# Kernel tuning notes

Hardware: AMD Instinct MI355X
Metric: run time of the kernel (lower is better)

The kernel has to match this reference:

```python
import jax, jax.numpy as jnp
import numpy as np

N, E, B = 100000, 3200000, 1024
D_LM, K, H, C, L = 1024, 128, 256, 40, 2
T = 0.1
LN_EPS = 1e-5


def _layernorm(x, g, b):
    m = x.mean(-1, keepdims=True)
    v = ((x - m) ** 2).mean(-1, keepdims=True)
    return (x - m) * jax.lax.rsqrt(v + LN_EPS) * g + b


def _gcn_conv(x, W, b, src, dst, norm, self_w):
    h = x @ W
    agg = jax.ops.segment_sum(h[src] * norm[:, None], dst, num_segments=N)
    return agg + h * self_w[:, None] + b


def setup_inputs() -> dict:
    key = jax.random.key(0)
    ks = jax.random.split(key, 20)
    s = 0.02
    rn = lambda k, shp: jax.random.normal(k, shp, jnp.float32) * s
    return {
        "hidden_embeds": jax.random.normal(ks[0], (L, N, D_LM), jnp.float32),
        "proj_W1": rn(ks[1], (L, D_LM, K)),
        "proj_b1": jnp.zeros((L, K), jnp.float32),
        "ln_g": jnp.ones((L, K), jnp.float32),
        "ln_b": jnp.zeros((L, K), jnp.float32),
        "proj_W2": rn(ks[2], (L, K, K)),
        "proj_b2": jnp.zeros((L, K), jnp.float32),
        "alphas": jnp.zeros((L,), jnp.float32),
        "gcn_W1": rn(ks[3], (L, K, H)),
        "gcn_b1": jnp.zeros((L, H), jnp.float32),
        "gcn_W2": rn(ks[4], (L, H, K)),
        "gcn_b2": jnp.zeros((L, K), jnp.float32),
        "clf_W": rn(ks[5], (2 * K, C)),
        "clf_b": jnp.zeros((C,), jnp.float32),
        "edge_index": jax.random.randint(ks[6], (2, E), 0, N, jnp.int64 if jax.config.jax_enable_x64 else jnp.int32),
        "mapping": jax.random.randint(ks[7], (B,), 0, N, jnp.int64 if jax.config.jax_enable_x64 else jnp.int32),
    }


def reference(hidden_embeds, proj_W1, proj_b1, ln_g, ln_b, proj_W2, proj_b2,
              alphas, gcn_W1, gcn_b1, gcn_W2, gcn_b2, clf_W, clf_b,
              edge_index, mapping):
    src, dst = edge_index[0], edge_index[1]
    ones = jnp.ones((E,), jnp.float32)
    # GCN normalization (self loops included): deg over dst + 1
    deg = jax.ops.segment_sum(ones, dst, num_segments=N) + 1.0
    dis = jax.lax.rsqrt(deg)
    norm = dis[src] * dis[dst]          # per-edge D^-1/2 A D^-1/2
    self_w = 1.0 / deg                  # self-loop weight dis[i]*dis[i]

    last = None
    for i in range(L):
        # projector: Linear -> LayerNorm -> ReLU -> Linear
        h = hidden_embeds[i] @ proj_W1[i] + proj_b1[i]
        h = jax.nn.relu(_layernorm(h, ln_g[i], ln_b[i]))
        h = h @ proj_W2[i] + proj_b2[i]
        if i > 0:
            a = jax.nn.sigmoid(alphas[i] / T)
            h = h * a + last * (1.0 - a)
        # 2-layer GCN encoder (dropout=0)
        z = jax.nn.relu(_gcn_conv(h, gcn_W1[i], gcn_b1[i], src, dst, norm, self_w))
        last = _gcn_conv(z, gcn_W2[i], gcn_b2[i], src, dst, norm, self_w)

    # custom_global_mean_pool: mean over {node} U {out-neighbors} U {in-neighbors}
    sum_n = (jax.ops.segment_sum(last[dst], src, num_segments=N)
             + jax.ops.segment_sum(last[src], dst, num_segments=N))
    cnt = (jax.ops.segment_sum(ones, src, num_segments=N)
           + jax.ops.segment_sum(ones, dst, num_segments=N))
    pooled = (last[mapping] + sum_n[mapping]) / (1.0 + cnt[mapping])[:, None]

    out = jnp.concatenate([last[mapping], pooled], axis=1)  # [B, 2K]
    return out @ clf_W + clf_b
```

## Files before the change

kernel.cpp:

```cpp
#include <hip/hip_runtime.h>
#include <hip/hip_bf16.h>
#include <math.h>

using short8 = __attribute__((ext_vector_type(8))) short;
using f32x4  = __attribute__((ext_vector_type(4))) float;

#define PSTRIDE 2048

__device__ __forceinline__ short f2bf(float f) {
    __hip_bfloat16 h = __float2bfloat16(f);
    return *reinterpret_cast<short*>(&h);
}


__global__ void map_scatter_k(const int* __restrict__ mapping, int* __restrict__ map_idx, int B)
{
    int b = blockIdx.x * blockDim.x + threadIdx.x;
    if (b < B) map_idx[mapping[b]] = b;
}

__launch_bounds__(1024)
__global__ void bin_count_k(const int* __restrict__ dst, int E, int* __restrict__ bin_cnt)
{
    __shared__ int h[4096];
    for (int i = threadIdx.x; i < 4096; i += 1024) h[i] = 0;
    __syncthreads();
    int base = blockIdx.x * 32768;
#pragma unroll
    for (int i = 0; i < 32; ++i) {
        int e = base + i * 1024 + threadIdx.x;
        if (e < E) atomicAdd(&h[dst[e] >> 5], 1);
    }
    __syncthreads();
    for (int i = threadIdx.x; i < 4096; i += 1024) {
        int c = h[i];
        if (c) atomicAdd(&bin_cnt[i], c);
    }
}

__launch_bounds__(1024)
__global__ void scan_bins_k(const int* __restrict__ cnt, int* __restrict__ off,
                            int* __restrict__ cur)
{
    __shared__ int wsum[16];
    int tid = threadIdx.x, lane = tid & 63, wid = tid >> 6;
    int4 v = ((const int4*)cnt)[tid];
    int s0 = v.x, s1 = s0 + v.y, s2 = s1 + v.z, s3 = s2 + v.w;
    int q = s3;
#pragma unroll
    for (int o = 1; o < 64; o <<= 1) { int t = __shfl_up(q, o); if (lane >= o) q += t; }
    if (lane == 63) wsum[wid] = q;
    __syncthreads();
    if (wid == 0) {
        int w = (lane < 16) ? wsum[lane] : 0;
#pragma unroll
        for (int o = 1; o < 16; o <<= 1) { int t = __shfl_up(w, o); if (lane >= o) w += t; }
        if (lane < 16) wsum[lane] = w;
    }
    __syncthreads();
    int base = (wid ? wsum[wid - 1] : 0) + q - s3;
    int4 o4; o4.x = base; o4.y = base + s0; o4.z = base + s1; o4.w = base + s2;
    ((int4*)off)[tid] = o4;
    ((int4*)cur)[tid] = o4;
    if (tid == 1023) off[4096] = base + s3;
}

__launch_bounds__(256)
__global__ void bin_scatter_k(const int* __restrict__ ei, int E,
                              const int* __restrict__ map_idx,
                              int* __restrict__ bin_cur, unsigned* __restrict__ pairs,
                              int* __restrict__ pcnt, int* __restrict__ pnb)
{
    int e = blockIdx.x * blockDim.x + threadIdx.x;
    if (e >= E) return;
    int s = ei[e];
    int d = ei[E + e];
    int p = atomicAdd(&bin_cur[d >> 5], 1);
    pairs[p] = (unsigned)s | ((unsigned)(d & 31) << 27);
    int ms = map_idx[s];
    if (ms >= 0) {
        int i = atomicAdd(&pcnt[ms], 1);
        if (i < PSTRIDE) pnb[ms * PSTRIDE + i] = d;
    }
    int md = map_idx[d];
    if (md >= 0) {
        int i = atomicAdd(&pcnt[md], 1);
        if (i < PSTRIDE) pnb[md * PSTRIDE + i] = s;
    }
}

__launch_bounds__(256)
__global__ void bin_csr_k(const unsigned* __restrict__ pairs, const int* __restrict__ bin_off,
                          int* __restrict__ csr_in, int* __restrict__ in_off,
                          float* __restrict__ dis, int N)
{
    __shared__ int lcnt[32];
    __shared__ int lofs[32];
    __shared__ int lcur[32];
    int b = blockIdx.x;
    int tid = threadIdx.x;
    if (tid < 32) lcnt[tid] = 0;
    __syncthreads();
    int beg = bin_off[b], end = bin_off[b + 1];
    for (int i = beg + tid; i < end; i += 256)
        atomicAdd(&lcnt[pairs[i] >> 27], 1);
    __syncthreads();
    if (tid == 0) {
        int run = beg;
#pragma unroll
        for (int j = 0; j < 32; ++j) { lofs[j] = run; lcur[j] = run; run += lcnt[j]; }
    }
    __syncthreads();
    int n0 = b * 32;
    if (tid < 32 && n0 + tid < N) {
        in_off[n0 + tid] = lofs[tid];
        float dg = (float)lcnt[tid] + 1.0f;
        dis[n0 + tid] = rsqrtf(dg);
    }
    if (b == gridDim.x - 1 && tid == 0) in_off[N] = end;
    for (int i = beg + tid; i < end; i += 256) {
        unsigned pr = pairs[i];
        int p = atomicAdd(&lcur[pr >> 27], 1);
        csr_in[p] = (int)(pr & 0x07FFFFFFu);
    }
}

__global__ void transpose_wb_k(const float* __restrict__ src, short* __restrict__ dst,
                               int LAY, int R, int Cc)
{
    int idx = blockIdx.x * blockDim.x + threadIdx.x;
    int tot = LAY * R * Cc;
    if (idx >= tot) return;
    int lay = idx / (R * Cc);
    int rem = idx - lay * R * Cc;
    int r = rem / Cc;
    int c = rem - r * Cc;
    dst[(size_t)lay * R * Cc + (size_t)c * R + r] = f2bf(src[idx]);
}

__launch_bounds__(256)
__global__ void proj_fused_k(const float* __restrict__ X,
                             const short* __restrict__ W1t,
                             const float* __restrict__ b1,
                             const float* __restrict__ lng,
                             const float* __restrict__ lnb,
                             const short* __restrict__ W2t,
                             const float* __restrict__ b2,
                             const float* __restrict__ alphas, int layer,
                             const float* __restrict__ last,
                             const float* __restrict__ dis,
                             short* __restrict__ out, int nrows)
{
    __shared__ short S[26624];

    const int tid  = threadIdx.x;
    const int lane = tid & 63;
    const int wave = tid >> 6;
    const int wr   = wave >> 1;
    const int wc   = wave & 1;
    const int g    = lane >> 4;
    const int lr   = lane & 15;
    const int row0 = blockIdx.x * 128;

    f32x4 acc[4][4];
#pragma unroll
    for (int fr = 0; fr < 4; ++fr)
#pragma unroll
        for (int fc = 0; fc < 4; ++fc) acc[fr][fc] = (f32x4){0.f, 0.f, 0.f, 0.f};

    const int xr   = tid >> 1;
    const int xc0  = (tid & 1) * 32;
    const bool xvalid = (row0 + xr) < nrows;
    const float* xbase = X + (size_t)(row0 + xr) * 1024 + xc0;
    const short* wbase = W1t + (size_t)(tid >> 1) * 1024 + (tid & 1) * 32;

    float4 xv[8];
    short8 wv[4];
    if (xvalid) {
#pragma unroll
        for (int m = 0; m < 8; ++m) xv[m] = *(const float4*)&xbase[m * 4];
    } else {
#pragma unroll
        for (int m = 0; m < 8; ++m) xv[m] = make_float4(0.f, 0.f, 0.f, 0.f);
    }
#pragma unroll
    for (int m = 0; m < 4; ++m) wv[m] = *(const short8*)&wbase[m * 8];

    for (int k0 = 0; k0 < 1024; k0 += 64) {
#pragma unroll
        for (int m = 0; m < 4; ++m) {
            short8 p;
            p[0]=f2bf(xv[2*m].x); p[1]=f2bf(xv[2*m].y); p[2]=f2bf(xv[2*m].z); p[3]=f2bf(xv[2*m].w);
            p[4]=f2bf(xv[2*m+1].x); p[5]=f2bf(xv[2*m+1].y); p[6]=f2bf(xv[2*m+1].z); p[7]=f2bf(xv[2*m+1].w);
            *(short8*)&S[xr * 72 + xc0 + m * 8] = p;
        }
#pragma unroll
        for (int m = 0; m < 4; ++m)
            *(short8*)&S[9216 + (tid >> 1) * 72 + (tid & 1) * 32 + m * 8] = wv[m];
        __syncthreads();

        if (k0 + 64 < 1024) {
            if (xvalid) {
                const float* xp = xbase + k0 + 64;
#pragma unroll
                for (int m = 0; m < 8; ++m) xv[m] = *(const float4*)&xp[m * 4];
            }
            const short* wp = wbase + k0 + 64;
#pragma unroll
            for (int m = 0; m < 4; ++m) wv[m] = *(const short8*)&wp[m * 8];
        }

#pragma unroll
        for (int kk = 0; kk < 64; kk += 32) {
            short8 a[4], b[4];
#pragma unroll
            for (int fr = 0; fr < 4; ++fr)
                a[fr] = *(short8*)&S[(wr * 64 + fr * 16 + lr) * 72 + kk + g * 8];
#pragma unroll
            for (int fc = 0; fc < 4; ++fc)
                b[fc] = *(short8*)&S[9216 + (wc * 64 + fc * 16 + lr) * 72 + kk + g * 8];
#pragma unroll
            for (int fr = 0; fr < 4; ++fr)
#pragma unroll
                for (int fc = 0; fc < 4; ++fc)
                    acc[fr][fc] = __builtin_amdgcn_mfma_f32_16x16x32_bf16(a[fr], b[fc], acc[fr][fc], 0, 0, 0);
        }
        __syncthreads();
    }

    float* P = (float*)&S[17408];
    {
        float b1v[4], gv[4], bv[4];
#pragma unroll
        for (int fc = 0; fc < 4; ++fc) {
            int col = wc * 64 + fc * 16 + lr;
            b1v[fc] = b1[col]; gv[fc] = lng[col]; bv[fc] = lnb[col];
        }
#pragma unroll
        for (int fr = 0; fr < 4; ++fr) {
#pragma unroll
            for (int j = 0; j < 4; ++j) {
                float s = 0.f, q = 0.f;
#pragma unroll
                for (int fc = 0; fc < 4; ++fc) {
                    float t = acc[fr][fc][j] + b1v[fc];
                    acc[fr][fc][j] = t;
                    s += t; q += t * t;
                }
#pragma unroll
                for (int m = 1; m < 16; m <<= 1) {
                    s += __shfl_xor(s, m);
                    q += __shfl_xor(q, m);
                }
                if (lr == 0) {
                    int row = wr * 64 + fr * 16 + 4 * g + j;
                    P[row * 4 + wc * 2]     = s;
                    P[row * 4 + wc * 2 + 1] = q;
                }
            }
        }
        __syncthreads();
#pragma unroll
        for (int fr = 0; fr < 4; ++fr) {
#pragma unroll
            for (int j = 0; j < 4; ++j) {
                int row = wr * 64 + fr * 16 + 4 * g + j;
                float s = P[row * 4 + 0] + P[row * 4 + 2];
                float q = P[row * 4 + 1] + P[row * 4 + 3];
                float mean = s * (1.0f / 128.0f);
                float var  = q * (1.0f / 128.0f) - mean * mean;
                float inv  = rsqrtf(var + 1e-5f);
#pragma unroll
                for (int fc = 0; fc < 4; ++fc) {
                    float h = fmaxf((acc[fr][fc][j] - mean) * inv * gv[fc] + bv[fc], 0.f);
                    S[row * 136 + wc * 64 + fc * 16 + lr] = f2bf(h);
                }
            }
        }
    }
    __syncthreads();

    f32x4 acc2[4][4];
#pragma unroll
    for (int fr = 0; fr < 4; ++fr)
#pragma unroll
        for (int fc = 0; fc < 4; ++fc) acc2[fr][fc] = (f32x4){0.f, 0.f, 0.f, 0.f};

    for (int k0 = 0; k0 < 128; k0 += 64) {
        {
            int c  = tid >> 1;
            int kb = (tid & 1) * 32;
            const short* wp = W2t + (size_t)c * 128 + k0 + kb;
#pragma unroll
            for (int m = 0; m < 4; ++m)
                *(short8*)&S[17408 + c * 72 + kb + m * 8] = *(const short8*)&wp[m * 8];
        }
        __syncthreads();
#pragma unroll
        for (int kk = 0; kk < 64; kk += 32) {
            short8 a[4], b[4];
#pragma unroll
            for (int fr = 0; fr < 4; ++fr)
                a[fr] = *(short8*)&S[(wr * 64 + fr * 16 + lr) * 136 + k0 + kk + g * 8];
#pragma unroll
            for (int fc = 0; fc < 4; ++fc)
                b[fc] = *(short8*)&S[17408 + (wc * 64 + fc * 16 + lr) * 72 + kk + g * 8];
#pragma unroll
            for (int fr = 0; fr < 4; ++fr)
#pragma unroll
                for (int fc = 0; fc < 4; ++fc)
                    acc2[fr][fc] = __builtin_amdgcn_mfma_f32_16x16x32_bf16(a[fr], b[fc], acc2[fr][fc], 0, 0, 0);
        }
        __syncthreads();
    }

    float b2v[4];
#pragma unroll
    for (int fc = 0; fc < 4; ++fc) b2v[fc] = b2[wc * 64 + fc * 16 + lr];
    float asig = 0.f, omas = 0.f;
    if (last) {
        float al = alphas[layer];
        asig = 1.0f / (1.0f + expf(-al * 10.0f));
        omas = 1.0f - asig;
    }
#pragma unroll
    for (int fr = 0; fr < 4; ++fr) {
#pragma unroll
        for (int j = 0; j < 4; ++j) {
            int gr = row0 + wr * 64 + fr * 16 + 4 * g + j;
            if (gr >= nrows) continue;
            float disr = dis[gr];
#pragma unroll
            for (int fc = 0; fc < 4; ++fc) {
                int col = wc * 64 + fc * 16 + lr;
                float o = acc2[fr][fc][j] + b2v[fc];
                if (last) o = asig * o + omas * last[(size_t)gr * 128 + col];
                out[(size_t)gr * 128 + col] = f2bf(o * disr);
            }
        }
    }
}

__launch_bounds__(256)
__global__ void gcn_mlp_k(const short* __restrict__ U,
                          const short* __restrict__ W1t,
                          const float* __restrict__ gb1,
                          const short* __restrict__ W2t,
                          const float* __restrict__ dis,
                          short* __restrict__ V, int M)
{
    __shared__ short S[35840];

    const int tid  = threadIdx.x;
    const int lane = tid & 63;
    const int wave = tid >> 6;
    const int g    = lane >> 4;
    const int lr   = lane & 15;
    const int m0   = blockIdx.x * 64;

#pragma unroll
    for (int it = 0; it < 4; ++it) {
        int i = tid + it * 256;
        int r = i >> 4;
        int c8 = i & 15;
        short8 v = {0,0,0,0,0,0,0,0};
        int gr = m0 + r;
        if (gr < M) v = *(const short8*)&U[(size_t)gr * 128 + c8 * 8];
        *(short8*)&S[r * 136 + c8 * 8] = v;
    }

    f32x4 acc[4][4];
#pragma unroll
    for (int fr = 0; fr < 4; ++fr)
#pragma unroll
        for (int fc = 0; fc < 4; ++fc) acc[fr][fc] = (f32x4){0.f, 0.f, 0.f, 0.f};

    for (int k0 = 0; k0 < 128; k0 += 64) {
#pragma unroll
        for (int it = 0; it < 8; ++it) {
            int i = tid + it * 256;
            int r = i >> 3;
            int c8 = i & 7;
            *(short8*)&S[17408 + r * 72 + c8 * 8] =
                *(const short8*)&W1t[(size_t)r * 128 + k0 + c8 * 8];
        }
        __syncthreads();
#pragma unroll
        for (int kk = 0; kk < 64; kk += 32) {
            short8 a[4], b[4];
#pragma unroll
            for (int fr = 0; fr < 4; ++fr)
                a[fr] = *(short8*)&S[(fr * 16 + lr) * 136 + k0 + kk + g * 8];
#pragma unroll
            for (int fc = 0; fc < 4; ++fc)
                b[fc] = *(short8*)&S[17408 + (wave * 64 + fc * 16 + lr) * 72 + kk + g * 8];
#pragma unroll
            for (int fr = 0; fr < 4; ++fr)
#pragma unroll
                for (int fc = 0; fc < 4; ++fc)
                    acc[fr][fc] = __builtin_amdgcn_mfma_f32_16x16x32_bf16(a[fr], b[fc], acc[fr][fc], 0, 0, 0);
        }
        __syncthreads();
    }

    {
        float bb[4];
#pragma unroll
        for (int fc = 0; fc < 4; ++fc) bb[fc] = gb1[wave * 64 + fc * 16 + lr];
#pragma unroll
        for (int fr = 0; fr < 4; ++fr) {
#pragma unroll
            for (int j = 0; j < 4; ++j) {
                int rloc = fr * 16 + 4 * g + j;
#pragma unroll
                for (int fc = 0; fc < 4; ++fc) {
                    float zv = fmaxf(acc[fr][fc][j] + bb[fc], 0.f);
                    S[rloc * 264 + wave * 64 + fc * 16 + lr] = f2bf(zv);
                }
            }
        }
    }

    f32x4 acc2[4][2];
#pragma unroll
    for (int fr = 0; fr < 4; ++fr) {
        acc2[fr][0] = (f32x4){0.f, 0.f, 0.f, 0.f};
        acc2[fr][1] = (f32x4){0.f, 0.f, 0.f, 0.f};
    }

    for (int k0 = 0; k0 < 256; k0 += 64) {
#pragma unroll
        for (int it = 0; it < 4; ++it) {
            int i = tid + it * 256;
            int r = i >> 3;
            int c8 = i & 7;
            *(short8*)&S[16896 + r * 72 + c8 * 8] =
                *(const short8*)&W2t[(size_t)r * 256 + k0 + c8 * 8];
        }
        __syncthreads();
#pragma unroll
        for (int kk = 0; kk < 64; kk += 32) {
            short8 a[4], b[2];
#pragma unroll
            for (int fr = 0; fr < 4; ++fr)
                a[fr] = *(short8*)&S[(fr * 16 + lr) * 264 + k0 + kk + g * 8];
#pragma unroll
            for (int fc = 0; fc < 2; ++fc)
                b[fc] = *(short8*)&S[16896 + (wave * 32 + fc * 16 + lr) * 72 + kk + g * 8];
#pragma unroll
            for (int fr = 0; fr < 4; ++fr)
#pragma unroll
                for (int fc = 0; fc < 2; ++fc)
                    acc2[fr][fc] = __builtin_amdgcn_mfma_f32_16x16x32_bf16(a[fr], b[fc], acc2[fr][fc], 0, 0, 0);
        }
        __syncthreads();
    }

#pragma unroll
    for (int fr = 0; fr < 4; ++fr) {
#pragma unroll
        for (int j = 0; j < 4; ++j) {
            int gr = m0 + fr * 16 + 4 * g + j;
            if (gr >= M) continue;
            float disr = dis[gr];
#pragma unroll
            for (int fc = 0; fc < 2; ++fc)
                V[(size_t)gr * 128 + wave * 32 + fc * 16 + lr] = f2bf(acc2[fr][fc][j] * disr);
        }
    }
}

template <bool OUT_BF16>
__launch_bounds__(256)
__global__ void agg_k(const unsigned* __restrict__ x, void* __restrict__ y,
                      const int* __restrict__ off, const int* __restrict__ csr,
                      const float* __restrict__ dis,
                      const float* __restrict__ bias, int N)
{
    int node = __builtin_amdgcn_readfirstlane(blockIdx.x * 4 + (threadIdx.x >> 6));
    if (node >= N) return;
    int lane = threadIdx.x & 63;
    int beg = off[node], end = off[node + 1];

    float ax0 = 0.f, ay0 = 0.f, ax1 = 0.f, ay1 = 0.f;
    float ax2 = 0.f, ay2 = 0.f, ax3 = 0.f, ay3 = 0.f;
    int e = beg;
    for (; e + 4 <= end; e += 4) {
        int s0 = csr[e], s1 = csr[e + 1], s2 = csr[e + 2], s3 = csr[e + 3];
        unsigned v0 = x[(size_t)s0 * 64 + lane];
        unsigned v1 = x[(size_t)s1 * 64 + lane];
        unsigned v2 = x[(size_t)s2 * 64 + lane];
        unsigned v3 = x[(size_t)s3 * 64 + lane];
        ax0 += __uint_as_float(v0 << 16);
        ay0 += __uint_as_float(v0 & 0xFFFF0000u);
        ax1 += __uint_as_float(v1 << 16);
        ay1 += __uint_as_float(v1 & 0xFFFF0000u);
        ax2 += __uint_as_float(v2 << 16);
        ay2 += __uint_as_float(v2 & 0xFFFF0000u);
        ax3 += __uint_as_float(v3 << 16);
        ay3 += __uint_as_float(v3 & 0xFFFF0000u);
    }
    for (; e < end; ++e) {
        int s = csr[e];
        unsigned v = x[(size_t)s * 64 + lane];
        ax0 += __uint_as_float(v << 16);
        ay0 += __uint_as_float(v & 0xFFFF0000u);
    }
    unsigned vo = x[(size_t)node * 64 + lane];
    float accx = ((ax0 + ax1) + (ax2 + ax3)) + __uint_as_float(vo << 16);
    float accy = ((ay0 + ay1) + (ay2 + ay3)) + __uint_as_float(vo & 0xFFFF0000u);

    float dn = dis[node];
    float rx = dn * accx;
    float ry = dn * accy;
    if (bias) { rx += bias[lane * 2]; ry += bias[lane * 2 + 1]; }
    if (OUT_BF16) {
        unsigned p = (unsigned)(unsigned short)f2bf(rx) | ((unsigned)(unsigned short)f2bf(ry) << 16);
        ((unsigned*)y)[(size_t)node * 64 + lane] = p;
    } else {
        *(float2*)&((float*)y)[(size_t)node * 128 + lane * 2] = make_float2(rx, ry);
    }
}

__launch_bounds__(128)
__global__ void pool_clf_k(const float* __restrict__ last, const int* __restrict__ mapping,
                           const int* __restrict__ map_idx,
                           const int* __restrict__ pcnt, const int* __restrict__ pnb,
                           const float* __restrict__ clfW, const float* __restrict__ clfb,
                           float* __restrict__ out, int C)
{
    int b = blockIdx.x;
    int tid = threadIdx.x;
    int n = mapping[b];
    int rep = map_idx[n];
    int cnt = pcnt[rep];
    int m = cnt < PSTRIDE ? cnt : PSTRIDE;

    float s = 0.f;
    const int* nb = pnb + (size_t)rep * PSTRIDE;
    for (int i = 0; i < m; ++i)
        s += last[(size_t)nb[i] * 128 + tid];

    float lv = last[(size_t)n * 128 + tid];
    float pooled = (lv + s) / (1.0f + (float)cnt);

    __shared__ float feat[256];
    feat[tid] = lv;
    feat[128 + tid] = pooled;
    __syncthreads();

    for (int c = tid; c < C; c += blockDim.x) {
        float o = clfb[c];
        for (int j = 0; j < 256; ++j) o = fmaf(feat[j], clfW[j * C + c], o);
        out[(size_t)b * C + c] = o;
    }
}

extern "C" void kernel_launch(void* const* d_in, const int* in_sizes, int n_in,
                              void* d_out, int out_size, void* d_ws, size_t ws_size,
                              hipStream_t stream)
{
    const float* hidden = (const float*)d_in[0];
    const float* pW1    = (const float*)d_in[1];
    const float* pb1    = (const float*)d_in[2];
    const float* lng    = (const float*)d_in[3];
    const float* lnb    = (const float*)d_in[4];
    const float* pW2    = (const float*)d_in[5];
    const float* pb2    = (const float*)d_in[6];
    const float* alphas = (const float*)d_in[7];
    const float* gW1    = (const float*)d_in[8];
    const float* gb1    = (const float*)d_in[9];
    const float* gW2    = (const float*)d_in[10];
    const float* gb2    = (const float*)d_in[11];
    const float* clfW   = (const float*)d_in[12];
    const float* clfb   = (const float*)d_in[13];
    const int*   ei     = (const int*)d_in[14];
    const int*   mapping= (const int*)d_in[15];

    const int L   = in_sizes[7];
    const int K   = in_sizes[2] / L;
    const int H   = in_sizes[9] / L;
    const int C   = in_sizes[13];
    const int DLM = in_sizes[1] / (L * K);
    const int N   = in_sizes[0] / (L * DLM);
    const int E   = in_sizes[14] / 2;
    const int B   = in_sizes[15];
    const int NBINS = (N + 31) / 32;

    char* ws = (char*)d_ws;
    size_t off = 0;
    auto carve = [&](size_t bytes) -> char* {
        char* p = ws + off;
        off += (bytes + 255) & ~(size_t)255;
        return p;
    };
    int*      map_idx = (int*)carve((size_t)N * 4);
    int*      pcnt    = (int*)carve((size_t)B * 4);
    int*      pnb     = (int*)carve((size_t)B * PSTRIDE * 4);
    int*      bin_cnt = (int*)carve(4096 * 4);
    int*      bin_off = (int*)carve(4097 * 4);
    int*      bin_cur = (int*)carve(4096 * 4);
    unsigned* pairs   = (unsigned*)carve((size_t)E * 4);
    int*      in_off  = (int*)carve((size_t)(N + 1) * 4);
    float*    dis     = (float*)carve((size_t)N * 4);
    int*      csr_in  = (int*)carve((size_t)E * 4);
    short*    bufA    = (short*)carve((size_t)N * K * 2);
    short*    bufU    = (short*)carve((size_t)N * K * 2);
    float*    bufLast = (float*)carve((size_t)N * K * 4);
    short*    w1t     = (short*)carve((size_t)L * K * DLM * 2);
    short*    w2t     = (short*)carve((size_t)L * K * K * 2);
    short*    gw1t    = (short*)carve((size_t)L * H * K * 2);
    short*    gw2t    = (short*)carve((size_t)L * K * H * 2);
    (void)ws_size; (void)n_in; (void)out_size;

    hipMemsetAsync(bin_cnt, 0, 4096 * 4, stream);
    hipMemsetAsync(map_idx, 0xFF, (size_t)N * 4, stream);
    hipMemsetAsync(pcnt, 0, (size_t)B * 4, stream);
    map_scatter_k<<<dim3((B + 255) / 256), 256, 0, stream>>>(mapping, map_idx, B);
    bin_count_k<<<dim3((E + 32767) / 32768), 1024, 0, stream>>>(ei + E, E, bin_cnt);
    scan_bins_k<<<dim3(1), 1024, 0, stream>>>(bin_cnt, bin_off, bin_cur);
    bin_scatter_k<<<dim3((E + 255) / 256), 256, 0, stream>>>(ei, E, map_idx, bin_cur,
                                                             pairs, pcnt, pnb);
    bin_csr_k<<<dim3(NBINS), 256, 0, stream>>>(pairs, bin_off, csr_in, in_off,
                                               dis, N);

    transpose_wb_k<<<dim3((L * DLM * K + 255) / 256), 256, 0, stream>>>(pW1, w1t, L, DLM, K);
    transpose_wb_k<<<dim3((L * K * K + 255) / 256), 256, 0, stream>>>(pW2, w2t, L, K, K);
    transpose_wb_k<<<dim3((L * K * H + 255) / 256), 256, 0, stream>>>(gW1, gw1t, L, K, H);
    transpose_wb_k<<<dim3((L * H * K + 255) / 256), 256, 0, stream>>>(gW2, gw2t, L, H, K);

    const int nblk64  = (N + 63) / 64;
    const int nblk128 = (N + 127) / 128;

    for (int i = 0; i < L; ++i) {
        proj_fused_k<<<dim3(nblk128), 256, 0, stream>>>(
            hidden + (size_t)i * N * DLM,
            w1t + (size_t)i * K * DLM,
            pb1 + (size_t)i * K,
            lng + (size_t)i * K,
            lnb + (size_t)i * K,
            w2t + (size_t)i * K * K,
            pb2 + (size_t)i * K,
            alphas, i,
            (i > 0) ? bufLast : nullptr,
            dis,
            bufA, N);

        agg_k<true><<<dim3((N + 3) / 4), 256, 0, stream>>>(
            (const unsigned*)bufA, bufU, in_off, csr_in, dis, nullptr, N);
        gcn_mlp_k<<<dim3(nblk64), 256, 0, stream>>>(
            bufU, gw1t + (size_t)i * H * K, gb1 + (size_t)i * H,
            gw2t + (size_t)i * K * H, dis, bufA, N);
        agg_k<false><<<dim3((N + 3) / 4), 256, 0, stream>>>(
            (const unsigned*)bufA, bufLast, in_off, csr_in, dis,
            gb2 + (size_t)i * K, N);
    }

    pool_clf_k<<<dim3(B), 128, 0, stream>>>(bufLast, mapping, map_idx, pcnt, pnb,
                                            clfW, clfb, (float*)d_out, C);
}
```

Before: 1.226 ms.

## Read weight fragments directly from global memory and shrink LDS for occupancy

The projector and GCN MLP kernels no longer stage weight tiles through shared memory. Each wave now loads its MFMA B fragments straight from global memory, which is expected to hit in cache because the weights are small and shared across blocks. This shrinks shared-memory footprints, drops several barriers per k-step, and adds a min-blocks hint of 4 to launch_bounds to raise occupancy. In exchange, the register prefetch of the next X tile in the projector is removed, so global load latency is no longer overlapped with compute, and weights are read redundantly per wave from L1/L2.

```diff
diff --git a/kernel.cpp b/kernel.cpp
--- a/kernel.cpp
+++ b/kernel.cpp
@@ -138,7 +138,7 @@
     dst[(size_t)lay * R * Cc + (size_t)c * R + r] = f2bf(src[idx]);
 }
 
-__launch_bounds__(256)
+__launch_bounds__(256, 4)
 __global__ void proj_fused_k(const float* __restrict__ X,
                              const short* __restrict__ W1t,
                              const float* __restrict__ b1,
@@ -151,7 +151,7 @@
                              const float* __restrict__ dis,
                              short* __restrict__ out, int nrows)
 {
-    __shared__ short S[26624];
+    __shared__ short S[18432];
 
     const int tid  = threadIdx.x;
     const int lane = tid & 63;
@@ -168,57 +168,45 @@
 #pragma unroll
         for (int fc = 0; fc < 4; ++fc) acc[fr][fc] = (f32x4){0.f, 0.f, 0.f, 0.f};
 
+    const short* w1base[4];
+#pragma unroll
+    for (int fc = 0; fc < 4; ++fc)
+        w1base[fc] = W1t + (size_t)(wc * 64 + fc * 16 + lr) * 1024 + g * 8;
+
     const int xr   = tid >> 1;
     const int xc0  = (tid & 1) * 32;
     const bool xvalid = (row0 + xr) < nrows;
     const float* xbase = X + (size_t)(row0 + xr) * 1024 + xc0;
-    const short* wbase = W1t + (size_t)(tid >> 1) * 1024 + (tid & 1) * 32;
-
-    float4 xv[8];
-    short8 wv[4];
-    if (xvalid) {
-#pragma unroll
-        for (int m = 0; m < 8; ++m) xv[m] = *(const float4*)&xbase[m * 4];
-    } else {
-#pragma unroll
-        for (int m = 0; m < 8; ++m) xv[m] = make_float4(0.f, 0.f, 0.f, 0.f);
-    }
-#pragma unroll
-    for (int m = 0; m < 4; ++m) wv[m] = *(const short8*)&wbase[m * 8];
 
     for (int k0 = 0; k0 < 1024; k0 += 64) {
-#pragma unroll
-        for (int m = 0; m < 4; ++m) {
-            short8 p;
-            p[0]=f2bf(xv[2*m].x); p[1]=f2bf(xv[2*m].y); p[2]=f2bf(xv[2*m].z); p[3]=f2bf(xv[2*m].w);
-            p[4]=f2bf(xv[2*m+1].x); p[5]=f2bf(xv[2*m+1].y); p[6]=f2bf(xv[2*m+1].z); p[7]=f2bf(xv[2*m+1].w);
-            *(short8*)&S[xr * 72 + xc0 + m * 8] = p;
-        }
-#pragma unroll
-        for (int m = 0; m < 4; ++m)
-            *(short8*)&S[9216 + (tid >> 1) * 72 + (tid & 1) * 32 + m * 8] = wv[m];
+        {
+            float4 v[8];
+            if (xvalid) {
+                const float* xp = xbase + k0;
+#pragma unroll
+                for (int m = 0; m < 8; ++m) v[m] = *(const float4*)&xp[m * 4];
+            } else {
+#pragma unroll
+                for (int m = 0; m < 8; ++m) v[m] = make_float4(0.f, 0.f, 0.f, 0.f);
+            }
+#pragma unroll
+            for (int m = 0; m < 4; ++m) {
+                short8 p;
+                p[0]=f2bf(v[2*m].x); p[1]=f2bf(v[2*m].y); p[2]=f2bf(v[2*m].z); p[3]=f2bf(v[2*m].w);
+                p[4]=f2bf(v[2*m+1].x); p[5]=f2bf(v[2*m+1].y); p[6]=f2bf(v[2*m+1].z); p[7]=f2bf(v[2*m+1].w);
+                *(short8*)&S[xr * 72 + xc0 + m * 8] = p;
+            }
+        }
         __syncthreads();
-
-        if (k0 + 64 < 1024) {
-            if (xvalid) {
-                const float* xp = xbase + k0 + 64;
-#pragma unroll
-                for (int m = 0; m < 8; ++m) xv[m] = *(const float4*)&xp[m * 4];
-            }
-            const short* wp = wbase + k0 + 64;
-#pragma unroll
-            for (int m = 0; m < 4; ++m) wv[m] = *(const short8*)&wp[m * 8];
-        }
-
 #pragma unroll
         for (int kk = 0; kk < 64; kk += 32) {
             short8 a[4], b[4];
 #pragma unroll
+            for (int fc = 0; fc < 4; ++fc)
+                b[fc] = *(const short8*)&w1base[fc][k0 + kk];
+#pragma unroll
             for (int fr = 0; fr < 4; ++fr)
                 a[fr] = *(short8*)&S[(wr * 64 + fr * 16 + lr) * 72 + kk + g * 8];
-#pragma unroll
-            for (int fc = 0; fc < 4; ++fc)
-                b[fc] = *(short8*)&S[9216 + (wc * 64 + fc * 16 + lr) * 72 + kk + g * 8];
 #pragma unroll
             for (int fr = 0; fr < 4; ++fr)
 #pragma unroll
@@ -286,32 +274,25 @@
 #pragma unroll
         for (int fc = 0; fc < 4; ++fc) acc2[fr][fc] = (f32x4){0.f, 0.f, 0.f, 0.f};
 
-    for (int k0 = 0; k0 < 128; k0 += 64) {
-        {
-            int c  = tid >> 1;
-            int kb = (tid & 1) * 32;
-            const short* wp = W2t + (size_t)c * 128 + k0 + kb;
-#pragma unroll
-            for (int m = 0; m < 4; ++m)
-                *(short8*)&S[17408 + c * 72 + kb + m * 8] = *(const short8*)&wp[m * 8];
-        }
-        __syncthreads();
-#pragma unroll
-        for (int kk = 0; kk < 64; kk += 32) {
-            short8 a[4], b[4];
-#pragma unroll
-            for (int fr = 0; fr < 4; ++fr)
-                a[fr] = *(short8*)&S[(wr * 64 + fr * 16 + lr) * 136 + k0 + kk + g * 8];
+    const short* w2base[4];
+#pragma unroll
+    for (int fc = 0; fc < 4; ++fc)
+        w2base[fc] = W2t + (size_t)(wc * 64 + fc * 16 + lr) * 128 + g * 8;
+
+#pragma unroll
+    for (int k0 = 0; k0 < 128; k0 += 32) {
+        short8 a[4], b[4];
+#pragma unroll
+        for (int fc = 0; fc < 4; ++fc)
+            b[fc] = *(const short8*)&w2base[fc][k0];
+#pragma unroll
+        for (int fr = 0; fr < 4; ++fr)
+            a[fr] = *(short8*)&S[(wr * 64 + fr * 16 + lr) * 136 + k0 + g * 8];
+#pragma unroll
+        for (int fr = 0; fr < 4; ++fr)
 #pragma unroll
             for (int fc = 0; fc < 4; ++fc)
-                b[fc] = *(short8*)&S[17408 + (wc * 64 + fc * 16 + lr) * 72 + kk + g * 8];
-#pragma unroll
-            for (int fr = 0; fr < 4; ++fr)
-#pragma unroll
-                for (int fc = 0; fc < 4; ++fc)
-                    acc2[fr][fc] = __builtin_amdgcn_mfma_f32_16x16x32_bf16(a[fr], b[fc], acc2[fr][fc], 0, 0, 0);
-        }
-        __syncthreads();
+                acc2[fr][fc] = __builtin_amdgcn_mfma_f32_16x16x32_bf16(a[fr], b[fc], acc2[fr][fc], 0, 0, 0);
     }
 
     float b2v[4];
@@ -341,7 +322,7 @@
     }
 }
 
-__launch_bounds__(256)
+__launch_bounds__(256, 4)
 __global__ void gcn_mlp_k(const short* __restrict__ U,
                           const short* __restrict__ W1t,
                           const float* __restrict__ gb1,
@@ -349,7 +330,7 @@
                           const float* __restrict__ dis,
                           short* __restrict__ V, int M)
 {
-    __shared__ short S[35840];
+    __shared__ short S[16896];
 
     const int tid  = threadIdx.x;
     const int lane = tid & 63;
@@ -368,6 +349,7 @@
         if (gr < M) v = *(const short8*)&U[(size_t)gr * 128 + c8 * 8];
         *(short8*)&S[r * 136 + c8 * 8] = v;
     }
+    __syncthreads();
 
     f32x4 acc[4][4];
 #pragma unroll
@@ -375,33 +357,27 @@
 #pragma unroll
         for (int fc = 0; fc < 4; ++fc) acc[fr][fc] = (f32x4){0.f, 0.f, 0.f, 0.f};
 
-    for (int k0 = 0; k0 < 128; k0 += 64) {
-#pragma unroll
-        for (int it = 0; it < 8; ++it) {
-            int i = tid + it * 256;
-            int r = i >> 3;
-            int c8 = i & 7;
-            *(short8*)&S[17408 + r * 72 + c8 * 8] =
-                *(const short8*)&W1t[(size_t)r * 128 + k0 + c8 * 8];
-        }
-        __syncthreads();
-#pragma unroll
-        for (int kk = 0; kk < 64; kk += 32) {
-            short8 a[4], b[4];
-#pragma unroll
-            for (int fr = 0; fr < 4; ++fr)
-                a[fr] = *(short8*)&S[(fr * 16 + lr) * 136 + k0 + kk + g * 8];
+    const short* w1base[4];
+#pragma unroll
+    for (int fc = 0; fc < 4; ++fc)
+        w1base[fc] = W1t + (size_t)(wave * 64 + fc * 16 + lr) * 128 + g * 8;
+
+#pragma unroll
+    for (int k0 = 0; k0 < 128; k0 += 32) {
+        short8 a[4], b[4];
+#pragma unroll
+        for (int fc = 0; fc < 4; ++fc)
+            b[fc] = *(const short8*)&w1base[fc][k0];
+#pragma unroll
+        for (int fr = 0; fr < 4; ++fr)
+            a[fr] = *(short8*)&S[(fr * 16 + lr) * 136 + k0 + g * 8];
+#pragma unroll
+        for (int fr = 0; fr < 4; ++fr)
 #pragma unroll
             for (int fc = 0; fc < 4; ++fc)
-                b[fc] = *(short8*)&S[17408 + (wave * 64 + fc * 16 + lr) * 72 + kk + g * 8];
-#pragma unroll
-            for (int fr = 0; fr < 4; ++fr)
-#pragma unroll
-                for (int fc = 0; fc < 4; ++fc)
-                    acc[fr][fc] = __builtin_amdgcn_mfma_f32_16x16x32_bf16(a[fr], b[fc], acc[fr][fc], 0, 0, 0);
-        }
-        __syncthreads();
-    }
+                acc[fr][fc] = __builtin_amdgcn_mfma_f32_16x16x32_bf16(a[fr], b[fc], acc[fr][fc], 0, 0, 0);
+    }
+    __syncthreads();
 
     {
         float bb[4];
@@ -420,6 +396,7 @@
             }
         }
     }
+    __syncthreads();
 
     f32x4 acc2[4][2];
 #pragma unroll
@@ -428,32 +405,25 @@
         acc2[fr][1] = (f32x4){0.f, 0.f, 0.f, 0.f};
     }
 
-    for (int k0 = 0; k0 < 256; k0 += 64) {
-#pragma unroll
-        for (int it = 0; it < 4; ++it) {
-            int i = tid + it * 256;
-            int r = i >> 3;
-            int c8 = i & 7;
-            *(short8*)&S[16896 + r * 72 + c8 * 8] =
-                *(const short8*)&W2t[(size_t)r * 256 + k0 + c8 * 8];
-        }
-        __syncthreads();
-#pragma unroll
-        for (int kk = 0; kk < 64; kk += 32) {
-            short8 a[4], b[2];
-#pragma unroll
-            for (int fr = 0; fr < 4; ++fr)
-                a[fr] = *(short8*)&S[(fr * 16 + lr) * 264 + k0 + kk + g * 8];
+    const short* w2base[2];
+#pragma unroll
+    for (int fc = 0; fc < 2; ++fc)
+        w2base[fc] = W2t + (size_t)(wave * 32 + fc * 16 + lr) * 256 + g * 8;
+
+#pragma unroll
+    for (int k0 = 0; k0 < 256; k0 += 32) {
+        short8 a[4], b[2];
+#pragma unroll
+        for (int fc = 0; fc < 2; ++fc)
+            b[fc] = *(const short8*)&w2base[fc][k0];
+#pragma unroll
+        for (int fr = 0; fr < 4; ++fr)
+            a[fr] = *(short8*)&S[(fr * 16 + lr) * 264 + k0 + g * 8];
+#pragma unroll
+        for (int fr = 0; fr < 4; ++fr)
 #pragma unroll
             for (int fc = 0; fc < 2; ++fc)
-                b[fc] = *(short8*)&S[16896 + (wave * 32 + fc * 16 + lr) * 72 + kk + g * 8];
-#pragma unroll
-            for (int fr = 0; fr < 4; ++fr)
-#pragma unroll
-                for (int fc = 0; fc < 2; ++fc)
-                    acc2[fr][fc] = __builtin_amdgcn_mfma_f32_16x16x32_bf16(a[fr], b[fc], acc2[fr][fc], 0, 0, 0);
-        }
-        __syncthreads();
+                acc2[fr][fc] = __builtin_amdgcn_mfma_f32_16x16x32_bf16(a[fr], b[fc], acc2[fr][fc], 0, 0, 0);
     }
 
 #pragma unroll
```

Result: no change. 1.249 ms (+1.9%).
